# Kernel tuning notes

Hardware: AMD Instinct MI355X
Metric: run time of the kernel (lower is better)

Reference implementation:

```python
import jax, jax.numpy as jnp
import numpy as np

ORD = 2  # matches EarthMoverLoss(ord=2)


def _lsa_square(cost):
    """Optimal linear sum assignment (minimize) on a square cost matrix.
    Shortest-augmenting-path algorithm, equivalent to
    scipy.optimize.linear_sum_assignment. Returns col4row: row i -> col4row[i].
    """
    n = cost.shape[0]
    u = np.zeros(n)
    v = np.zeros(n)
    path = np.full(n, -1, dtype=np.int64)
    col4row = np.full(n, -1, dtype=np.int64)
    row4col = np.full(n, -1, dtype=np.int64)
    rows = np.arange(n)
    for cur_row in range(n):
        min_val = 0.0
        i = cur_row
        SR = np.zeros(n, dtype=bool)   # scanned rows
        SC = np.zeros(n, dtype=bool)   # scanned cols
        shortest = np.full(n, np.inf)  # shortest path cost to each col
        sink = -1
        while sink == -1:
            SR[i] = True
            cols = np.flatnonzero(~SC)
            r = min_val + cost[i, cols] - u[i] - v[cols]
            upd = r < shortest[cols]
            cu = cols[upd]
            shortest[cu] = r[upd]
            path[cu] = i
            k = np.argmin(shortest[cols])
            j = cols[k]
            min_val = shortest[j]
            if np.isinf(min_val):
                raise ValueError('infeasible cost matrix')
            SC[j] = True
            if row4col[j] == -1:
                sink = j
            else:
                i = row4col[j]
        # dual variable update
        u[cur_row] += min_val
        others = SR & (rows != cur_row)
        u[others] += min_val - shortest[col4row[others]]
        v[SC] -= min_val - shortest[SC]
        # augment along the alternating path
        j = sink
        while True:
            i = path[j]
            row4col[j] = i
            col4row[i], j = j, col4row[i]
            if i == cur_row:
                break
    return col4row


def _batched_assignment(x, y):
    """Per-sample Euclidean cdist + Hungarian; mirrors the torch module's
    detached CPU/scipy path. Returns [B, N] int permutation of y per sample."""
    xn = np.asarray(jax.device_get(x), dtype=np.float64)
    yn = np.asarray(jax.device_get(y), dtype=np.float64)
    perms = []
    for b in range(xn.shape[0]):
        d2 = ((xn[b, :, None, :] - yn[b, None, :, :]) ** 2).sum(-1)  # [N, N]
        perms.append(_lsa_square(np.sqrt(d2)))
    return jnp.asarray(np.stack(perms))  # [B, N]


def setup_inputs() -> dict:
    key = jax.random.key(0)
    k1, k2 = jax.random.split(key)
    pred = jax.random.normal(k1, (8, 256, 3), dtype=jnp.float32)
    label = jax.random.normal(k2, (8, 256, 3), dtype=jnp.float32)
    return {"pred": pred, "label": label}


def reference(pred, label):
    # Hungarian matching on detached values (scipy returns ind1 = arange for
    # a square cost matrix, so only label is permuted).
    perm = _batched_assignment(pred, label)                      # [B, N]
    matched_y = jnp.take_along_axis(label, perm[:, :, None], axis=1)  # [B, N, D]
    # mean over batch and points of the ord-2 vector norm along coord dim
    return jnp.mean(jnp.linalg.norm(pred - matched_y, ord=ORD, axis=2))
```

## Files before the change

### kernel.cpp

```cpp
#include <hip/hip_runtime.h>
#include <math.h>

#define NPTS 256
#define NB 8
#define CPL 4

#if __has_builtin(__builtin_amdgcn_sqrtf)
#define FSQRT __builtin_amdgcn_sqrtf
#else
#define FSQRT sqrtf
#endif

__device__ __forceinline__ double dist3d(double ax, double ay, double az,
                                         double bx, double by, double bz) {
#pragma clang fp contract(off)
  double d0 = ax - bx;
  double d1 = ay - by;
  double d2 = az - bz;
  double s = d0 * d0;
  s = s + d1 * d1;
  s = s + d2 * d2;
  return sqrt(s);
}

__device__ __forceinline__ float distf(float ax, float ay, float az,
                                       float bx, float by, float bz) {
  float d0 = ax - bx, d1 = ay - by, d2 = az - bz;
  return FSQRT(d0 * d0 + d1 * d1 + d2 * d2);
}

__device__ __forceinline__ unsigned wave_min_u32(unsigned x) {
  int v = (int)x;
  v = min(v ^ 0, v);
  unsigned r = x;
  r = min(r, (unsigned)__builtin_amdgcn_update_dpp((int)r, (int)r, 0x111, 0xF, 0xF, false));
  r = min(r, (unsigned)__builtin_amdgcn_update_dpp((int)r, (int)r, 0x112, 0xF, 0xF, false));
  r = min(r, (unsigned)__builtin_amdgcn_update_dpp((int)r, (int)r, 0x114, 0xF, 0xF, false));
  r = min(r, (unsigned)__builtin_amdgcn_update_dpp((int)r, (int)r, 0x118, 0xF, 0xF, false));
  r = min(r, (unsigned)__builtin_amdgcn_update_dpp((int)r, (int)r, 0x142, 0xF, 0xF, false));
  r = min(r, (unsigned)__builtin_amdgcn_update_dpp((int)r, (int)r, 0x143, 0xF, 0xF, false));
  return (unsigned)__builtin_amdgcn_readlane((int)r, 63);
}

__global__ __launch_bounds__(64) void emd_lsa_kernel(
    const float* __restrict__ pred, const float* __restrict__ label,
    double* __restrict__ partial) {
  __shared__ float4 rowd[NPTS];
  __shared__ float ys0[NPTS], ys1[NPTS], ys2[NPTS];
  __shared__ float short_l[NPTS];
  __shared__ int path_l[NPTS];
  __shared__ int c4r_l[NPTS];
  __shared__ int r4c_l[NPTS];
  __shared__ int sr_l[NPTS];
  __shared__ int bcfr[NPTS];

  const int lane = threadIdx.x;
  const int b = blockIdx.x;
  const float* xg = pred + (size_t)b * NPTS * 3;
  const float* yg = label + (size_t)b * NPTS * 3;

  float yc0[CPL], yc1[CPL], yc2[CPL];
  float v_reg[CPL];
  int r4c_reg[CPL];

#pragma unroll
  for (int c = 0; c < CPL; ++c) {
    int j = lane * CPL + c;
    rowd[j] = make_float4(xg[j * 3 + 0], xg[j * 3 + 1], xg[j * 3 + 2], 0.0f);
    float t0 = yg[j * 3 + 0], t1 = yg[j * 3 + 1], t2 = yg[j * 3 + 2];
    ys0[j] = t0; ys1[j] = t1; ys2[j] = t2;
    yc0[c] = t0; yc1[c] = t1; yc2[c] = t2;
    c4r_l[j] = -1;
    r4c_l[j] = -1;
    bcfr[j] = 0x7FFFFFFF;
  }
  __syncthreads();

  float cmin[CPL];
  int imin[CPL];
#pragma unroll
  for (int c = 0; c < CPL; ++c) { cmin[c] = 3.4e38f; imin[c] = -1; }
  for (int i = 0; i < NPTS; ++i) {
    float4 rd = rowd[i];
#pragma unroll
    for (int c = 0; c < CPL; ++c) {
      float d = distf(rd.x, rd.y, rd.z, yc0[c], yc1[c], yc2[c]);
      bool upd = d < cmin[c];
      cmin[c] = upd ? d : cmin[c];
      imin[c] = upd ? i : imin[c];
    }
  }
#pragma unroll
  for (int c = 0; c < CPL; ++c) {
    v_reg[c] = cmin[c];
    atomicMin(&bcfr[imin[c]], lane * CPL + c);
  }
  __syncthreads();
#pragma unroll
  for (int c = 0; c < CPL; ++c) {
    int j = lane * CPL + c;
    if (bcfr[imin[c]] == j) {
      r4c_l[j] = imin[c];
      c4r_l[imin[c]] = j;
    }
  }
  __syncthreads();
#pragma unroll
  for (int c = 0; c < CPL; ++c) r4c_reg[c] = r4c_l[lane * CPL + c];
  __syncthreads();

  const float INF = 3.4e38f;

  for (int cur_row = 0; cur_row < NPTS; ++cur_row) {
    if (c4r_l[cur_row] != -1) continue;

    float shortest[CPL];
    int path_r[CPL];
    int scn[CPL];
#pragma unroll
    for (int c = 0; c < CPL; ++c) {
      shortest[c] = INF;
      path_r[c] = -1;
      scn[c] = 0;
      sr_l[lane * CPL + c] = 0;
    }
    __syncthreads();

    float min_val = 0.0f;
    int i = cur_row;
    int sink = -1;

    while (true) {
      sr_l[i] = 1;
      float4 rd = rowd[i];
      float base = min_val - rd.w;
      unsigned lkey = 0xFFFFFFFFu;
#pragma unroll
      for (int c = 0; c < CPL; ++c) {
        float cst = distf(rd.x, rd.y, rd.z, yc0[c], yc1[c], yc2[c]);
        float r = (base + cst) - v_reg[c];
        bool upd = (r < shortest[c]) && !scn[c];
        shortest[c] = upd ? r : shortest[c];
        path_r[c] = upd ? i : path_r[c];
        float snn = fmaxf(shortest[c], 0.0f);
        unsigned k = (__float_as_uint(snn) & 0xFFFFFF00u) | (unsigned)(lane * CPL + c);
        k = scn[c] ? 0xFFFFFFFFu : k;
        lkey = min(lkey, k);
      }
      unsigned best = wave_min_u32(lkey);
      int jstar = (int)(best & 0xFFu);
      int csel = jstar & (CPL - 1);
      int owner = jstar >> 2;

      if (owner == lane) {
        scn[csel] = 1;
        short_l[jstar] = shortest[csel];
        path_l[jstar] = path_r[csel];
      }
      float slo = (csel & 1) ? shortest[1] : shortest[0];
      float shi = (csel & 1) ? shortest[3] : shortest[2];
      float ssel = (csel & 2) ? shi : slo;
      int rlo = (csel & 1) ? r4c_reg[1] : r4c_reg[0];
      int rhi = (csel & 1) ? r4c_reg[3] : r4c_reg[2];
      int rsel = (csel & 2) ? rhi : rlo;
      min_val = __shfl(ssel, owner);
      int nr = __shfl(rsel, owner);
      if (nr < 0) { sink = jstar; break; }
      i = nr;
    }
    __syncthreads();

#pragma unroll
    for (int c = 0; c < CPL; ++c) {
      int row = lane * CPL + c;
      if (sr_l[row]) {
        float du = (row == cur_row) ? min_val : (min_val - short_l[c4r_l[row]]);
        rowd[row].w += du;
      }
      if (scn[c]) v_reg[c] -= min_val - shortest[c];
    }
    __syncthreads();

    if (lane == 0) {
      int jj = sink;
      while (true) {
        int ii = path_l[jj];
        r4c_l[jj] = ii;
        int tmp = c4r_l[ii];
        c4r_l[ii] = jj;
        jj = tmp;
        if (ii == cur_row) break;
      }
    }
    __syncthreads();
#pragma unroll
    for (int c = 0; c < CPL; ++c) r4c_reg[c] = r4c_l[lane * CPL + c];
    __syncthreads();
  }

  double s = 0.0;
#pragma unroll
  for (int c = 0; c < CPL; ++c) {
    int row = lane * CPL + c;
    int j = c4r_l[row];
    float4 rd = rowd[row];
    s += dist3d((double)rd.x, (double)rd.y, (double)rd.z,
                (double)ys0[j], (double)ys1[j], (double)ys2[j]);
  }
  for (int m = 1; m < 64; m <<= 1) s += __shfl_xor(s, m);
  if (lane == 0) partial[b] = s;
}

__global__ void emd_finalize_kernel(const double* __restrict__ partial,
                                    float* __restrict__ out) {
  if (threadIdx.x == 0 && blockIdx.x == 0) {
    double s = 0.0;
    for (int b = 0; b < NB; ++b) s += partial[b];
    out[0] = (float)(s / (double)(NB * NPTS));
  }
}

extern "C" void kernel_launch(void* const* d_in, const int* in_sizes, int n_in,
                              void* d_out, int out_size, void* d_ws, size_t ws_size,
                              hipStream_t stream) {
  const float* pred = (const float*)d_in[0];
  const float* label = (const float*)d_in[1];
  double* partial = (double*)d_ws;
  emd_lsa_kernel<<<NB, 64, 0, stream>>>(pred, label, partial);
  emd_finalize_kernel<<<1, 64, 0, stream>>>(partial, (float*)d_out);
}
```

Measured before the change: 1.321 ms.

## Add auction-style augmenting row reduction before shortest-path phase

Adds two rounds of augmenting row reduction (as in the LAPJV algorithm). Each free row finds its best and second-best reduced-cost columns, adjusts column duals and takes the column, possibly displacing another row. Free rows are then collected into a compacted queue, so the Dijkstra-style augmentation loop visits only the rows still unassigned. This aims to cut the number of costly shortest-path searches, at the cost of added wave reductions and shared-memory traffic, plus a risk of float-precision differences in which assignment is reached.

```diff
diff --git a/kernel.cpp b/kernel.cpp
--- a/kernel.cpp
+++ b/kernel.cpp
@@ -30,8 +30,6 @@
 }
 
 __device__ __forceinline__ unsigned wave_min_u32(unsigned x) {
-  int v = (int)x;
-  v = min(v ^ 0, v);
   unsigned r = x;
   r = min(r, (unsigned)__builtin_amdgcn_update_dpp((int)r, (int)r, 0x111, 0xF, 0xF, false));
   r = min(r, (unsigned)__builtin_amdgcn_update_dpp((int)r, (int)r, 0x112, 0xF, 0xF, false));
@@ -40,6 +38,19 @@
   r = min(r, (unsigned)__builtin_amdgcn_update_dpp((int)r, (int)r, 0x142, 0xF, 0xF, false));
   r = min(r, (unsigned)__builtin_amdgcn_update_dpp((int)r, (int)r, 0x143, 0xF, 0xF, false));
   return (unsigned)__builtin_amdgcn_readlane((int)r, 63);
+}
+
+__device__ __forceinline__ float sel4_shfl(const float a[CPL], int c, int owner) {
+  float lo = (c & 1) ? a[1] : a[0];
+  float hi = (c & 1) ? a[3] : a[2];
+  float s = (c & 2) ? hi : lo;
+  return __shfl(s, owner);
+}
+__device__ __forceinline__ int sel4i_shfl(const int a[CPL], int c, int owner) {
+  int lo = (c & 1) ? a[1] : a[0];
+  int hi = (c & 1) ? a[3] : a[2];
+  int s = (c & 2) ? hi : lo;
+  return __shfl(s, owner);
 }
 
 __global__ __launch_bounds__(64) void emd_lsa_kernel(
@@ -53,6 +64,7 @@
   __shared__ int r4c_l[NPTS];
   __shared__ int sr_l[NPTS];
   __shared__ int bcfr[NPTS];
+  __shared__ int fq[NPTS];
 
   const int lane = threadIdx.x;
   const int b = blockIdx.x;
@@ -109,10 +121,99 @@
   for (int c = 0; c < CPL; ++c) r4c_reg[c] = r4c_l[lane * CPL + c];
   __syncthreads();
 
+  int nf;
+  {
+    int4 cc = *(int4*)&c4r_l[lane * CPL];
+    bool f0 = cc.x < 0, f1 = cc.y < 0, f2 = cc.z < 0, f3 = cc.w < 0;
+    unsigned long long b0 = __ballot(f0), b1 = __ballot(f1);
+    unsigned long long b2 = __ballot(f2), b3 = __ballot(f3);
+    unsigned long long lt = (1ull << lane) - 1ull;
+    int off = __popcll(b0 & lt) + __popcll(b1 & lt) + __popcll(b2 & lt) + __popcll(b3 & lt);
+    if (f0) fq[off++] = lane * CPL + 0;
+    if (f1) fq[off++] = lane * CPL + 1;
+    if (f2) fq[off++] = lane * CPL + 2;
+    if (f3) fq[off++] = lane * CPL + 3;
+    nf = __popcll(b0) + __popcll(b1) + __popcll(b2) + __popcll(b3);
+  }
+  __syncthreads();
+
+  for (int rnd = 0; rnd < 2; ++rnd) {
+    int nf_new = 0, k = 0, guard = 0;
+    while (k < nf && ++guard <= 1024) {
+      int i = fq[k]; k++;
+      float4 rd = rowd[i];
+      float rr[CPL];
+      unsigned kk[CPL];
+      unsigned lk = 0xFFFFFFFFu;
+#pragma unroll
+      for (int c = 0; c < CPL; ++c) {
+        float d = distf(rd.x, rd.y, rd.z, yc0[c], yc1[c], yc2[c]);
+        rr[c] = d - v_reg[c];
+        kk[c] = (__float_as_uint(fmaxf(rr[c], 0.0f)) & 0xFFFFFF00u) |
+                (unsigned)(lane * CPL + c);
+        lk = min(lk, kk[c]);
+      }
+      unsigned k1 = wave_min_u32(lk);
+      int j1 = (int)(k1 & 0xFFu), c1 = j1 & (CPL - 1), o1 = j1 >> 2;
+      float u1 = sel4_shfl(rr, c1, o1);
+      int i0 = sel4i_shfl(r4c_reg, c1, o1);
+      unsigned lk2 = 0xFFFFFFFFu;
+#pragma unroll
+      for (int c = 0; c < CPL; ++c) {
+        unsigned kc = (lane * CPL + c == j1) ? 0xFFFFFFFFu : kk[c];
+        lk2 = min(lk2, kc);
+      }
+      unsigned k2 = wave_min_u32(lk2);
+      int j2 = (int)(k2 & 0xFFu);
+      float u2 = sel4_shfl(rr, j2 & (CPL - 1), j2 >> 2);
+
+      bool strict = u1 < u2;
+      int jT = j1, iT = i0;
+      if (strict) {
+        if (lane == o1) v_reg[c1] -= (u2 - u1);
+      } else if (i0 >= 0) {
+        jT = j2;
+        iT = sel4i_shfl(r4c_reg, j2 & (CPL - 1), j2 >> 2);
+      }
+      if (lane == (jT >> 2)) { r4c_reg[jT & (CPL - 1)] = i; r4c_l[jT] = i; }
+      if (lane == 0) {
+        c4r_l[i] = jT;
+        if (iT >= 0) c4r_l[iT] = -1;
+        rowd[i].w = strict ? u2 : u1;
+      }
+      if (iT >= 0) {
+        if (strict) {
+          k--;
+          if (lane == 0) fq[k] = iT;
+        } else {
+          if (lane == 0) fq[nf_new] = iT;
+          nf_new++;
+        }
+      }
+    }
+    nf = nf_new;
+    __syncthreads();
+  }
+
+  {
+    int4 cc = *(int4*)&c4r_l[lane * CPL];
+    bool f0 = cc.x < 0, f1 = cc.y < 0, f2 = cc.z < 0, f3 = cc.w < 0;
+    unsigned long long b0 = __ballot(f0), b1 = __ballot(f1);
+    unsigned long long b2 = __ballot(f2), b3 = __ballot(f3);
+    unsigned long long lt = (1ull << lane) - 1ull;
+    int off = __popcll(b0 & lt) + __popcll(b1 & lt) + __popcll(b2 & lt) + __popcll(b3 & lt);
+    if (f0) fq[off++] = lane * CPL + 0;
+    if (f1) fq[off++] = lane * CPL + 1;
+    if (f2) fq[off++] = lane * CPL + 2;
+    if (f3) fq[off++] = lane * CPL + 3;
+    nf = __popcll(b0) + __popcll(b1) + __popcll(b2) + __popcll(b3);
+  }
+  __syncthreads();
+
   const float INF = 3.4e38f;
 
-  for (int cur_row = 0; cur_row < NPTS; ++cur_row) {
-    if (c4r_l[cur_row] != -1) continue;
+  for (int t = 0; t < nf; ++t) {
+    int cur_row = fq[t];
 
     float shortest[CPL];
     int path_r[CPL];
@@ -157,14 +258,8 @@
         short_l[jstar] = shortest[csel];
         path_l[jstar] = path_r[csel];
       }
-      float slo = (csel & 1) ? shortest[1] : shortest[0];
-      float shi = (csel & 1) ? shortest[3] : shortest[2];
-      float ssel = (csel & 2) ? shi : slo;
-      int rlo = (csel & 1) ? r4c_reg[1] : r4c_reg[0];
-      int rhi = (csel & 1) ? r4c_reg[3] : r4c_reg[2];
-      int rsel = (csel & 2) ? rhi : rlo;
-      min_val = __shfl(ssel, owner);
-      int nr = __shfl(rsel, owner);
+      min_val = sel4_shfl(shortest, csel, owner);
+      int nr = sel4i_shfl(r4c_reg, csel, owner);
       if (nr < 0) { sink = jstar; break; }
       i = nr;
     }
```

Measured after the change: 2.236 ms. +69.3%, slower.

## Shorten Hungarian inner loop with in-lane argmin, readlane broadcasts and row prefetch

Applied to the files above, without the earlier changes.

Each lane now reduces its four columns to one key and carries the matching row4col, shortest and path values along, so the wave min is followed by scalar readlane broadcasts instead of dynamic-index selects and shuffles. The next row's coordinates are read from LDS speculatively before the wave reduction, which takes that load off the serial critical path. Free rows are compacted into a queue with ballots so already-assigned rows are skipped without a loop check. Every lane now writes short_l and path_l with the same uniform value, which adds some redundant LDS stores.

```diff
diff --git a/kernel.cpp b/kernel.cpp
--- a/kernel.cpp
+++ b/kernel.cpp
@@ -3,7 +3,6 @@
 
 #define NPTS 256
 #define NB 8
-#define CPL 4
 
 #if __has_builtin(__builtin_amdgcn_sqrtf)
 #define FSQRT __builtin_amdgcn_sqrtf
@@ -30,8 +29,6 @@
 }
 
 __device__ __forceinline__ unsigned wave_min_u32(unsigned x) {
-  int v = (int)x;
-  v = min(v ^ 0, v);
   unsigned r = x;
   r = min(r, (unsigned)__builtin_amdgcn_update_dpp((int)r, (int)r, 0x111, 0xF, 0xF, false));
   r = min(r, (unsigned)__builtin_amdgcn_update_dpp((int)r, (int)r, 0x112, 0xF, 0xF, false));
@@ -53,132 +50,138 @@
   __shared__ int r4c_l[NPTS];
   __shared__ int sr_l[NPTS];
   __shared__ int bcfr[NPTS];
+  __shared__ int fq[NPTS];
 
   const int lane = threadIdx.x;
   const int b = blockIdx.x;
   const float* xg = pred + (size_t)b * NPTS * 3;
   const float* yg = label + (size_t)b * NPTS * 3;
 
-  float yc0[CPL], yc1[CPL], yc2[CPL];
-  float v_reg[CPL];
-  int r4c_reg[CPL];
-
-#pragma unroll
-  for (int c = 0; c < CPL; ++c) {
-    int j = lane * CPL + c;
-    rowd[j] = make_float4(xg[j * 3 + 0], xg[j * 3 + 1], xg[j * 3 + 2], 0.0f);
-    float t0 = yg[j * 3 + 0], t1 = yg[j * 3 + 1], t2 = yg[j * 3 + 2];
-    ys0[j] = t0; ys1[j] = t1; ys2[j] = t2;
-    yc0[c] = t0; yc1[c] = t1; yc2[c] = t2;
-    c4r_l[j] = -1;
-    r4c_l[j] = -1;
-    bcfr[j] = 0x7FFFFFFF;
-  }
-  __syncthreads();
-
-  float cmin[CPL];
-  int imin[CPL];
-#pragma unroll
-  for (int c = 0; c < CPL; ++c) { cmin[c] = 3.4e38f; imin[c] = -1; }
+  const int cid0 = lane * 4, cid1 = cid0 + 1, cid2 = cid0 + 2, cid3 = cid0 + 3;
+
+  float q0x, q0y, q0z, q1x, q1y, q1z, q2x, q2y, q2z, q3x, q3y, q3z;
+  float vv0, vv1, vv2, vv3;
+  int rc0, rc1, rc2, rc3;
+
+#define INITC(c) { int j = cid##c; \
+    rowd[j] = make_float4(xg[j*3+0], xg[j*3+1], xg[j*3+2], 0.0f); \
+    float t0 = yg[j*3+0], t1 = yg[j*3+1], t2 = yg[j*3+2]; \
+    ys0[j] = t0; ys1[j] = t1; ys2[j] = t2; \
+    q##c##x = t0; q##c##y = t1; q##c##z = t2; \
+    c4r_l[j] = -1; r4c_l[j] = -1; bcfr[j] = 0x7FFFFFFF; }
+  INITC(0) INITC(1) INITC(2) INITC(3)
+#undef INITC
+  __syncthreads();
+
+  float mm0 = 3.4e38f, mm1 = 3.4e38f, mm2 = 3.4e38f, mm3 = 3.4e38f;
+  int im0 = -1, im1 = -1, im2 = -1, im3 = -1;
   for (int i = 0; i < NPTS; ++i) {
     float4 rd = rowd[i];
-#pragma unroll
-    for (int c = 0; c < CPL; ++c) {
-      float d = distf(rd.x, rd.y, rd.z, yc0[c], yc1[c], yc2[c]);
-      bool upd = d < cmin[c];
-      cmin[c] = upd ? d : cmin[c];
-      imin[c] = upd ? i : imin[c];
-    }
-  }
-#pragma unroll
-  for (int c = 0; c < CPL; ++c) {
-    v_reg[c] = cmin[c];
-    atomicMin(&bcfr[imin[c]], lane * CPL + c);
-  }
-  __syncthreads();
-#pragma unroll
-  for (int c = 0; c < CPL; ++c) {
-    int j = lane * CPL + c;
-    if (bcfr[imin[c]] == j) {
-      r4c_l[j] = imin[c];
-      c4r_l[imin[c]] = j;
-    }
-  }
-  __syncthreads();
-#pragma unroll
-  for (int c = 0; c < CPL; ++c) r4c_reg[c] = r4c_l[lane * CPL + c];
+#define CRED(c) { float d = distf(rd.x, rd.y, rd.z, q##c##x, q##c##y, q##c##z); \
+    bool u_ = d < mm##c; mm##c = u_ ? d : mm##c; im##c = u_ ? i : im##c; }
+    CRED(0) CRED(1) CRED(2) CRED(3)
+#undef CRED
+  }
+  vv0 = mm0; vv1 = mm1; vv2 = mm2; vv3 = mm3;
+  atomicMin(&bcfr[im0], cid0);
+  atomicMin(&bcfr[im1], cid1);
+  atomicMin(&bcfr[im2], cid2);
+  atomicMin(&bcfr[im3], cid3);
+  __syncthreads();
+  if (bcfr[im0] == cid0) { r4c_l[cid0] = im0; c4r_l[im0] = cid0; }
+  if (bcfr[im1] == cid1) { r4c_l[cid1] = im1; c4r_l[im1] = cid1; }
+  if (bcfr[im2] == cid2) { r4c_l[cid2] = im2; c4r_l[im2] = cid2; }
+  if (bcfr[im3] == cid3) { r4c_l[cid3] = im3; c4r_l[im3] = cid3; }
+  __syncthreads();
+  rc0 = r4c_l[cid0]; rc1 = r4c_l[cid1]; rc2 = r4c_l[cid2]; rc3 = r4c_l[cid3];
+
+  int nf;
+  {
+    int4 cc = *(int4*)&c4r_l[cid0];
+    bool f0 = cc.x < 0, f1 = cc.y < 0, f2 = cc.z < 0, f3 = cc.w < 0;
+    unsigned long long b0 = __ballot(f0), b1 = __ballot(f1);
+    unsigned long long b2 = __ballot(f2), b3 = __ballot(f3);
+    unsigned long long lt = (1ull << lane) - 1ull;
+    int off = __popcll(b0 & lt) + __popcll(b1 & lt) + __popcll(b2 & lt) + __popcll(b3 & lt);
+    if (f0) fq[off++] = cid0;
+    if (f1) fq[off++] = cid1;
+    if (f2) fq[off++] = cid2;
+    if (f3) fq[off++] = cid3;
+    nf = __popcll(b0) + __popcll(b1) + __popcll(b2) + __popcll(b3);
+  }
   __syncthreads();
 
   const float INF = 3.4e38f;
 
-  for (int cur_row = 0; cur_row < NPTS; ++cur_row) {
-    if (c4r_l[cur_row] != -1) continue;
-
-    float shortest[CPL];
-    int path_r[CPL];
-    int scn[CPL];
-#pragma unroll
-    for (int c = 0; c < CPL; ++c) {
-      shortest[c] = INF;
-      path_r[c] = -1;
-      scn[c] = 0;
-      sr_l[lane * CPL + c] = 0;
-    }
+  for (int t = 0; t < nf; ++t) {
+    int cur_row = fq[t];
+
+    float sh0 = INF, sh1 = INF, sh2 = INF, sh3 = INF;
+    int pp0 = -1, pp1 = -1, pp2 = -1, pp3 = -1;
+    int sc0 = 0, sc1 = 0, sc2 = 0, sc3 = 0;
+    *(int4*)&sr_l[cid0] = make_int4(0, 0, 0, 0);
     __syncthreads();
 
     float min_val = 0.0f;
     int i = cur_row;
     int sink = -1;
+    float xi, yi, zi, ui;
+    { float4 r0 = rowd[cur_row]; xi = r0.x; yi = r0.y; zi = r0.z; ui = r0.w; }
 
     while (true) {
       sr_l[i] = 1;
-      float4 rd = rowd[i];
-      float base = min_val - rd.w;
-      unsigned lkey = 0xFFFFFFFFu;
-#pragma unroll
-      for (int c = 0; c < CPL; ++c) {
-        float cst = distf(rd.x, rd.y, rd.z, yc0[c], yc1[c], yc2[c]);
-        float r = (base + cst) - v_reg[c];
-        bool upd = (r < shortest[c]) && !scn[c];
-        shortest[c] = upd ? r : shortest[c];
-        path_r[c] = upd ? i : path_r[c];
-        float snn = fmaxf(shortest[c], 0.0f);
-        unsigned k = (__float_as_uint(snn) & 0xFFFFFF00u) | (unsigned)(lane * CPL + c);
-        k = scn[c] ? 0xFFFFFFFFu : k;
-        lkey = min(lkey, k);
-      }
+      float base = min_val - ui;
+      unsigned k0, k1, k2, k3;
+#define SSTEP(c) { float d = distf(xi, yi, zi, q##c##x, q##c##y, q##c##z); \
+      float r = (base + d) - vv##c; \
+      bool u_ = (r < sh##c) && (sc##c == 0); \
+      sh##c = u_ ? r : sh##c; \
+      pp##c = u_ ? i : pp##c; \
+      unsigned kk = (__float_as_uint(fmaxf(sh##c, 0.0f)) & 0xFFFFFF00u) | (unsigned)cid##c; \
+      k##c = sc##c ? 0xFFFFFFFFu : kk; }
+      SSTEP(0) SSTEP(1) SSTEP(2) SSTEP(3)
+#undef SSTEP
+      bool t01 = k1 < k0;
+      unsigned ka = t01 ? k1 : k0; int na = t01 ? rc1 : rc0;
+      float ea = t01 ? sh1 : sh0;  int pa = t01 ? pp1 : pp0;
+      bool t23 = k3 < k2;
+      unsigned kb = t23 ? k3 : k2; int nb2 = t23 ? rc3 : rc2;
+      float eb = t23 ? sh3 : sh2;  int pb = t23 ? pp3 : pp2;
+      bool tf = kb < ka;
+      unsigned lkey = tf ? kb : ka; int nl = tf ? nb2 : na;
+      float el = tf ? eb : ea;     int pl = tf ? pb : pa;
+
+      float4 pre = rowd[nl < 0 ? 0 : nl];
+
       unsigned best = wave_min_u32(lkey);
       int jstar = (int)(best & 0xFFu);
-      int csel = jstar & (CPL - 1);
-      int owner = jstar >> 2;
-
-      if (owner == lane) {
-        scn[csel] = 1;
-        short_l[jstar] = shortest[csel];
-        path_l[jstar] = path_r[csel];
-      }
-      float slo = (csel & 1) ? shortest[1] : shortest[0];
-      float shi = (csel & 1) ? shortest[3] : shortest[2];
-      float ssel = (csel & 2) ? shi : slo;
-      int rlo = (csel & 1) ? r4c_reg[1] : r4c_reg[0];
-      int rhi = (csel & 1) ? r4c_reg[3] : r4c_reg[2];
-      int rsel = (csel & 2) ? rhi : rlo;
-      min_val = __shfl(ssel, owner);
-      int nr = __shfl(rsel, owner);
+      int w = jstar >> 2;
+
+      int nr = __builtin_amdgcn_readlane(nl, w);
+      min_val = __int_as_float(__builtin_amdgcn_readlane(__float_as_int(el), w));
+      int pj = __builtin_amdgcn_readlane(pl, w);
+
+      short_l[jstar] = min_val;
+      path_l[jstar] = pj;
+      sc0 |= (cid0 == jstar); sc1 |= (cid1 == jstar);
+      sc2 |= (cid2 == jstar); sc3 |= (cid3 == jstar);
+
       if (nr < 0) { sink = jstar; break; }
       i = nr;
+      xi = __int_as_float(__builtin_amdgcn_readlane(__float_as_int(pre.x), w));
+      yi = __int_as_float(__builtin_amdgcn_readlane(__float_as_int(pre.y), w));
+      zi = __int_as_float(__builtin_amdgcn_readlane(__float_as_int(pre.z), w));
+      ui = __int_as_float(__builtin_amdgcn_readlane(__float_as_int(pre.w), w));
     }
     __syncthreads();
 
-#pragma unroll
-    for (int c = 0; c < CPL; ++c) {
-      int row = lane * CPL + c;
-      if (sr_l[row]) {
-        float du = (row == cur_row) ? min_val : (min_val - short_l[c4r_l[row]]);
-        rowd[row].w += du;
-      }
-      if (scn[c]) v_reg[c] -= min_val - shortest[c];
-    }
+#define DUALU(c) { int row = cid##c; \
+      if (sr_l[row]) { \
+        float du = (row == cur_row) ? min_val : (min_val - short_l[c4r_l[row]]); \
+        rowd[row].w += du; } \
+      if (sc##c) vv##c -= min_val - sh##c; }
+    DUALU(0) DUALU(1) DUALU(2) DUALU(3)
+#undef DUALU
     __syncthreads();
 
     if (lane == 0) {
@@ -193,20 +196,16 @@
       }
     }
     __syncthreads();
-#pragma unroll
-    for (int c = 0; c < CPL; ++c) r4c_reg[c] = r4c_l[lane * CPL + c];
+    rc0 = r4c_l[cid0]; rc1 = r4c_l[cid1]; rc2 = r4c_l[cid2]; rc3 = r4c_l[cid3];
     __syncthreads();
   }
 
   double s = 0.0;
-#pragma unroll
-  for (int c = 0; c < CPL; ++c) {
-    int row = lane * CPL + c;
-    int j = c4r_l[row];
-    float4 rd = rowd[row];
-    s += dist3d((double)rd.x, (double)rd.y, (double)rd.z,
-                (double)ys0[j], (double)ys1[j], (double)ys2[j]);
-  }
+#define FIN(c) { int row = cid##c; int j = c4r_l[row]; float4 rd = rowd[row]; \
+    s += dist3d((double)rd.x, (double)rd.y, (double)rd.z, \
+                (double)ys0[j], (double)ys1[j], (double)ys2[j]); }
+  FIN(0) FIN(1) FIN(2) FIN(3)
+#undef FIN
   for (int m = 1; m < 64; m <<= 1) s += __shfl_xor(s, m);
   if (lane == 0) partial[b] = s;
 }
```

Measured after the change: 1.420 ms. +7.5%, slower.
